# Kernel optimization log

Hardware: AMD Instinct MI355X
Metric: run time of the kernel (lower is better)

The kernel has to match this reference:

```python
import jax, jax.numpy as jnp
import numpy as np

N, C_IN, T, V = 64, 64, 64, 25
C_OUT = 64
DK = DV = 16
NH = 8
DKH, DVH = DK // NH, DV // NH
KT = 9
EPS = 1e-5


def make_pe(channel, joint_num, time_len):
    # temporal positional encoding: position index = frame id, repeated per joint
    pos = np.repeat(np.arange(time_len), joint_num).astype(np.float32)[:, None]
    pe = np.zeros((time_len * joint_num, channel), np.float32)
    div = np.exp(np.arange(0, channel, 2).astype(np.float32) * -(np.log(10000.0) / channel))
    pe[:, 0::2] = np.sin(pos * div)
    pe[:, 1::2] = np.cos(pos * div)
    return jnp.asarray(pe.reshape(time_len, joint_num, channel).transpose(2, 0, 1)[None])  # (1,C,time,joint)


def setup_inputs():
    key = jax.random.key(0)
    ks = jax.random.split(key, 17)
    rn = lambda k, s, sc=0.05: jax.random.normal(k, s, jnp.float32) * sc
    return {
        'x': jax.random.normal(ks[0], (N, C_IN, T, V), jnp.float32),
        'pe': make_pe(C_IN, V, 64),
        'data_bn_g': 1.0 + rn(ks[1], (C_IN * V,)),
        'data_bn_b': rn(ks[2], (C_IN * V,)),
        'qkv_w': rn(ks[3], (3 * DK + DV, C_IN), 0.1),
        'qkv_b': rn(ks[4], (3 * DK + DV,)),
        'attn_w': rn(ks[5], (DV, DV), 0.1),
        'attn_b': rn(ks[6], (DV,)),
        'tcn_w': rn(ks[7], (C_OUT - DV, C_IN, KT, 1), 0.05),
        'tcn_b': rn(ks[8], (C_OUT - DV,)),
        'tcn_bn_g': 1.0 + rn(ks[9], (C_OUT - DV,)),
        'tcn_bn_b': rn(ks[10], (C_OUT - DV,)),
        'fc1_w': rn(ks[11], (C_OUT // 2, C_OUT), 0.1),
        'fc1_b': rn(ks[12], (C_OUT // 2,)),
        'fc2_w': rn(ks[13], (C_OUT, C_OUT // 2), 0.1),
        'fc2_b': rn(ks[14], (C_OUT,)),
        'bn_g': 1.0 + rn(ks[15], (C_OUT,)),
        'bn_b': rn(ks[16], (C_OUT,)),
    }


def _bn_eval(x, g, b, axis=1):
    # eval-mode BatchNorm with running_mean=0, running_var=1
    shape = [1] * x.ndim
    shape[axis] = -1
    scale = g / jnp.sqrt(1.0 + EPS)
    return x * scale.reshape(shape) + b.reshape(shape)


def _qkv_heads(x2d, qkv_w, qkv_b):
    # x2d: (B, C, T); 1x1 conv == channel matmul; split q/k/g/v, g is projected but unused
    qkv = jnp.einsum('oc,bct->bot', qkv_w, x2d) + qkv_b[None, :, None]
    q, k, _g, v = jnp.split(qkv, [DK, 2 * DK, 3 * DK], axis=1)
    B = x2d.shape[0]
    split = lambda z, ch: z.reshape(B, NH, ch // NH, -1)  # (B, Nh, chh, T)
    q = split(q, DK) * (DKH ** -0.5)
    return q, split(k, DK), split(v, DV)


def reference(x, pe, data_bn_g, data_bn_b, qkv_w, qkv_b, attn_w, attn_b,
              tcn_w, tcn_b, tcn_bn_g, tcn_bn_b, fc1_w, fc1_b, fc2_w, fc2_b, bn_g, bn_b):
    y = x + pe[:, :, :T]                                 # positional encoding (N,C,T,V)
    x_sum = x
    # data_bn over flattened (C*V) channels
    xb = x.transpose(0, 1, 3, 2).reshape(N, C_IN * V, T)
    xb = _bn_eval(xb, data_bn_g, data_bn_b)
    xn = xb.reshape(N, C_IN, V, T).transpose(0, 1, 3, 2)  # (N,C,T,V)
    # fold joints into batch: (N*V, C, T)
    xf = xn.transpose(0, 3, 1, 2).reshape(N * V, C_IN, T)
    yf = y.transpose(0, 3, 1, 2).reshape(N * V, C_IN, T)
    fq, fk, fv = _qkv_heads(xf, qkv_w, qkv_b)
    pq, pk, _ = _qkv_heads(yf, qkv_w, qkv_b)
    mu_q = fq.mean(-1, keepdims=True)                     # (B,H,dkh,1)
    fqc = fq - mu_q
    logits_pos = jnp.einsum('bhcs,bhct->bhst', pq, pk)    # (B,H,T,T)
    pairwise = jnp.einsum('bhcs,bhct->bhst', fqc, fk)     # (B,H,T,T)
    unary = jnp.einsum('bhcs,bhct->bhst', mu_q, fk)       # (B,H,1,T)
    weights = jnp.tanh(pairwise + logits_pos) + jnp.tanh(unary + logits_pos)
    ao = jnp.einsum('bhst,bhct->bhsc', weights, fv)       # (B,H,T,dvh)
    # (B,H,1,T,dvh) -> permute(0,1,4,2,3) -> combine heads -> (B, DV, T)
    ao = ao.transpose(0, 1, 3, 2).reshape(N * V, DV, T)
    ao = jnp.einsum('oc,bct->bot', attn_w, ao) + attn_b[None, :, None]
    ao = ao.reshape(N, V, DV, T).transpose(0, 2, 3, 1)    # (N, DV, T, V)
    # temporal conv branch (Unit2D: conv(k=9 temporal) + eval BN)
    tc = jax.lax.conv_general_dilated(x_sum, tcn_w, (1, 1), ((KT // 2, KT // 2), (0, 0)),
                                      dimension_numbers=('NCHW', 'OIHW', 'NCHW'))
    tc = tc + tcn_b[None, :, None, None]
    tc = _bn_eval(tc, tcn_bn_g, tcn_bn_b)
    result = jnp.concatenate([tc, ao], axis=1) + x_sum    # residual (down is None)
    # SE-style channel gating
    se = result.mean(axis=(2, 3))                         # (N, C_OUT)
    gate = jax.nn.sigmoid(jax.nn.relu(se @ fc1_w.T + fc1_b) @ fc2_w.T + fc2_b)
    result = result * gate[:, :, None, None] + result
    result = _bn_eval(result, bn_g, bn_b)
    return jax.nn.relu(result)
```

## Files before the change

### kernel.cpp

```cpp
#include <hip/hip_runtime.h>
#include <hip/hip_bf16.h>
#include <math.h>

#define TV_ 1600
#define SCALE_K 2.885390081777927f
#define RS2_ 0.70710678118654752f

typedef __attribute__((ext_vector_type(8))) short bf16x8;
typedef __attribute__((ext_vector_type(4))) float f32x4;
typedef __attribute__((ext_vector_type(2))) __fp16 h2f;

union F4H { float4 f; h2f h[4]; };
union F2H { float2 f; h2f h[2]; };

__device__ __forceinline__ float tanh4(float y) {
    float e = __builtin_amdgcn_exp2f(y);
    float r = __builtin_amdgcn_rcpf(e + 1.f);
    return __builtin_fmaf(-2.f, r, 1.f);
}

__device__ __forceinline__ float dot2f(h2f a, h2f b, float c) {
    return __builtin_amdgcn_fdot2(a, b, c, false);
}

__device__ __forceinline__ ushort f2bf(float f) {
    __hip_bfloat16 h = __float2bfloat16(f);
    return *(ushort*)&h;
}
__device__ __forceinline__ float bf2f(ushort u) {
    uint w = ((uint)u) << 16;
    return __uint_as_float(w);
}

__global__ __launch_bounds__(256) void t1_kernel(
    const float* __restrict__ x, const float* __restrict__ pe,
    const float* __restrict__ tcn_w, const float* __restrict__ tg,
    const float* __restrict__ qkv_w, const float* __restrict__ qkv_b,
    const float* __restrict__ dbg, const float* __restrict__ dbb,
    ushort* __restrict__ rt, float* __restrict__ Sp, float* __restrict__ Tt,
    ushort* __restrict__ wb, ushort* __restrict__ wq, float* __restrict__ qb,
    ushort* __restrict__ pet, float* __restrict__ dbs)
{
    const int tid = threadIdx.x;
    const int bx = blockIdx.x, by = blockIdx.y;

    if (bx == 25) {
        #pragma unroll 1
        for (int j = 0; j < 9; ++j) {
            int idx = by * 256 + tid + j * 16384;
            if (idx < 27648) {
                int oc = idx / 576, kk = idx - oc * 576;
                int kt = kk >> 6, ci = kk & 63;
                float a = tg[oc] * rsqrtf(1.f + 1e-5f);
                wb[idx] = f2bf(tcn_w[(oc * 64 + ci) * 9 + kt] * a);
            } else if (idx < 32768) {
                int i2 = idx - 27648;
                int r = i2 >> 6, c = i2 & 63;
                int src; float sc;
                if (r < 16)      { src = r;      sc = RS2_; }
                else if (r < 32) { src = r;      sc = SCALE_K; }
                else if (r < 48) { src = r + 16; sc = 1.f; }
                else if (r < 64) { src = r - 48; sc = RS2_; }
                else             { src = r - 48; sc = SCALE_K; }
                wq[i2] = f2bf(qkv_w[src * 64 + c] * sc);
            } else if (idx < 32848) {
                int r = idx - 32768;
                int src; float sc;
                if (r < 16)      { src = r;      sc = RS2_; }
                else if (r < 32) { src = r;      sc = SCALE_K; }
                else if (r < 48) { src = r + 16; sc = 1.f; }
                else if (r < 64) { src = r - 48; sc = RS2_; }
                else             { src = r - 48; sc = SCALE_K; }
                qb[r] = qkv_b[src] * sc;
            } else if (idx < 135248) {
                int i3 = idx - 32848;
                int ci = i3 / 1600, tv = i3 - ci * 1600;
                pet[tv * 64 + ci] = f2bf(pe[ci * 1600 + tv]);
            } else if (idx < 138448) {
                int i4 = idx - 135248;
                int v = i4 >> 7, r = i4 & 127;
                if (r < 64) dbs[i4] = dbg[r * 25 + v] * rsqrtf(1.f + 1e-5f);
                else        dbs[i4] = dbb[(r - 64) * 25 + v];
            }
        }
        return;
    }
    if (bx == 26) {
        const int n = by;
        #pragma unroll
        for (int it = 0; it < 2; ++it) {
            int item = tid + it * 256;
            int ci = item >> 3, slot = item & 7;
            int t = (slot < 4) ? slot : (56 + slot);
            const float* xp = x + (n * 64 + ci) * TV_ + t * 25;
            float s = 0.f;
            #pragma unroll
            for (int v = 0; v < 25; ++v) s += xp[v];
            Tt[(n * 64 + ci) * 8 + slot] = s;
        }
        return;
    }

    __shared__ ushort smt[64 * 66];
    __shared__ float sps[64 * 65];
    const int tv0 = bx * 64;
    const int n = by;
    const int tvl = tid & 63, cig = tid >> 6;
    const int tv = tv0 + tvl;

    #pragma unroll
    for (int k = 0; k < 16; ++k) {
        int ci = cig * 16 + k;
        float xv = x[(n * 64 + ci) * TV_ + tv];
        smt[tvl * 66 + ci] = f2bf(xv);
        sps[ci * 65 + tvl] = xv;
    }
    __syncthreads();

    {
        const int c = tid >> 2, qr = tid & 3;
        float s = 0.f;
        #pragma unroll
        for (int i = 0; i < 16; ++i) s += sps[c * 65 + qr * 16 + i];
        s += __shfl_xor(s, 1);
        s += __shfl_xor(s, 2);
        if (qr == 0) Sp[(n * 25 + bx) * 64 + c] = s;
    }

    #pragma unroll
    for (int j = 0; j < 8; ++j) {
        int chunk = tid + j * 256;
        int tvr = chunk >> 5, p = chunk & 31;
        uint val = *(const uint*)&smt[tvr * 66 + p * 2];
        *(uint*)&rt[(n * TV_ + tv0 + tvr) * 64 + p * 2] = val;
    }
}

__global__ __launch_bounds__(256, 5) void score_kernel(
    const ushort* __restrict__ rt, const ushort* __restrict__ pet,
    const float* __restrict__ dbs,
    const ushort* __restrict__ wq, const float* __restrict__ qb,
    const float* __restrict__ attn_w, const float* __restrict__ attn_b,
    float* __restrict__ aoc, float* __restrict__ sep)
{
    __shared__ float sm[5856];
    ushort* smu = (ushort*)sm;
    const int MU_ = 1056;
    const int FK2 = 1120, PK2 = 1664, FV2 = 2208, PQ2 = 2752, FQ2 = 3296;
    const int AO2 = 3840;
    const int UN_ = 5312;

    const int b = blockIdx.x;
    const int l = b >> 3;
    const int n = (b & 7) * 8 + l / 25;
    const int v = l % 25;
    const int tid = threadIdx.x;

    const int lane = tid & 63, wave = tid >> 6;
    const int m16 = lane & 15, q = lane >> 4;

    {
        const int part = tid & 7;
        const int ci0 = part * 8;
        float sc8[8], sh8[8];
        *(float4*)&sc8[0] = *(const float4*)&dbs[v * 128 + ci0];
        *(float4*)&sc8[4] = *(const float4*)&dbs[v * 128 + ci0 + 4];
        *(float4*)&sh8[0] = *(const float4*)&dbs[v * 128 + 64 + ci0];
        *(float4*)&sh8[4] = *(const float4*)&dbs[v * 128 + 64 + ci0 + 4];
        #pragma unroll
        for (int j = 0; j < 2; ++j) {
            int t = (tid + j * 256) >> 3;
            uint4 xr = *(const uint4*)&rt[(n * TV_ + t * 25 + v) * 64 + ci0];
            uint4 pr = *(const uint4*)&pet[(t * 25 + v) * 64 + ci0];
            const ushort* xu = (const ushort*)&xr;
            const ushort* pu = (const ushort*)&pr;
            ushort xs[8], ys[8];
            #pragma unroll
            for (int i = 0; i < 8; ++i) {
                float xf = bf2f(xu[i]);
                xs[i] = f2bf(xf * sc8[i] + sh8[i]);
                ys[i] = f2bf(xf + bf2f(pu[i]));
            }
            *(uint4*)&smu[t * 72 + ci0] = *(uint4*)xs;
            *(uint4*)&smu[4608 + t * 72 + ci0] = *(uint4*)ys;
        }
    }
    __syncthreads();

    f32x4 acc[5];
    #pragma unroll
    for (int mt = 0; mt < 5; ++mt) acc[mt] = (f32x4){0.f, 0.f, 0.f, 0.f};
    #pragma unroll
    for (int kt = 0; kt < 2; ++kt) {
        const int koff = kt * 32 + q * 8;
        bf16x8 bx = *(const bf16x8*)&smu[(wave * 16 + m16) * 72 + koff];
        bf16x8 by = *(const bf16x8*)&smu[4608 + (wave * 16 + m16) * 72 + koff];
        #pragma unroll
        for (int mt = 0; mt < 5; ++mt) {
            bf16x8 a = *(const bf16x8*)&wq[(mt * 16 + m16) * 64 + koff];
            acc[mt] = __builtin_amdgcn_mfma_f32_16x16x32_bf16(a, (mt < 3) ? bx : by, acc[mt], 0, 0, 0);
        }
    }
    __syncthreads();

    {
        const int t = wave * 16 + m16;
        #pragma unroll
        for (int r = 0; r < 4; ++r)
            sm[(q * 4 + r) * 66 + t] = acc[0][r] + qb[q * 4 + r];
        const int p0 = (2 * q) * 68 + t, p1 = (2 * q + 1) * 68 + t;
        *(h2f*)&sm[FK2 + p0] = __builtin_amdgcn_cvt_pkrtz(acc[1][0] + qb[16 + 4 * q],     acc[1][1] + qb[16 + 4 * q + 1]);
        *(h2f*)&sm[FK2 + p1] = __builtin_amdgcn_cvt_pkrtz(acc[1][2] + qb[16 + 4 * q + 2], acc[1][3] + qb[16 + 4 * q + 3]);
        *(h2f*)&sm[FV2 + p0] = __builtin_amdgcn_cvt_pkrtz(acc[2][0] + qb[32 + 4 * q],     acc[2][1] + qb[32 + 4 * q + 1]);
        *(h2f*)&sm[FV2 + p1] = __builtin_amdgcn_cvt_pkrtz(acc[2][2] + qb[32 + 4 * q + 2], acc[2][3] + qb[32 + 4 * q + 3]);
        *(h2f*)&sm[PQ2 + p0] = __builtin_amdgcn_cvt_pkrtz(acc[3][0] + qb[48 + 4 * q],     acc[3][1] + qb[48 + 4 * q + 1]);
        *(h2f*)&sm[PQ2 + p1] = __builtin_amdgcn_cvt_pkrtz(acc[3][2] + qb[48 + 4 * q + 2], acc[3][3] + qb[48 + 4 * q + 3]);
        *(h2f*)&sm[PK2 + p0] = __builtin_amdgcn_cvt_pkrtz(acc[4][0] + qb[64 + 4 * q],     acc[4][1] + qb[64 + 4 * q + 1]);
        *(h2f*)&sm[PK2 + p1] = __builtin_amdgcn_cvt_pkrtz(acc[4][2] + qb[64 + 4 * q + 2], acc[4][3] + qb[64 + 4 * q + 3]);
    }
    __syncthreads();

    if (tid < 64) {
        int ch = tid & 15, qq = tid >> 4;
        float s = 0.f;
        #pragma unroll
        for (int t = 0; t < 16; ++t) s += sm[ch * 66 + qq * 16 + t];
        sm[MU_ + qq * 16 + ch] = s;
    }
    __syncthreads();
    if (tid < 16) {
        float mval = (sm[MU_ + tid] + sm[MU_ + 16 + tid] + sm[MU_ + 32 + tid] + sm[MU_ + 48 + tid]) * (1.f / 64.f);
        sm[MU_ + tid] = mval;
    }
    __syncthreads();

    #pragma unroll
    for (int e = 0; e < 2; ++e) {
        int idx = tid * 2 + e;
        int s = idx >> 3, h = idx & 7;
        float a = sm[(2 * h) * 66 + s] - sm[MU_ + 2 * h];
        float c = sm[(2 * h + 1) * 66 + s] - sm[MU_ + 2 * h + 1];
        *(h2f*)&sm[FQ2 + h * 68 + s] = __builtin_amdgcn_cvt_pkrtz(a, c);
    }
    {
        const int h = tid & 7, tt = tid >> 3;
        h2f mp = __builtin_amdgcn_cvt_pkrtz(sm[MU_ + 2 * h], sm[MU_ + 2 * h + 1]);
        sm[UN_ + h * 68 + tt]      = dot2f(mp, *(const h2f*)&sm[FK2 + h * 68 + tt], 0.f);
        sm[UN_ + h * 68 + tt + 32] = dot2f(mp, *(const h2f*)&sm[FK2 + h * 68 + tt + 32], 0.f);
    }
    __syncthreads();

    {
        const int h = tid & 7, sp = tid >> 3;
        const int hb = h * 68;
        F2H fqp, pqp;
        fqp.f = *(const float2*)&sm[FQ2 + hb + 2 * sp];
        pqp.f = *(const float2*)&sm[PQ2 + hb + 2 * sp];
        const h2f fq0 = fqp.h[0], fq1 = fqp.h[1];
        const h2f pq0 = pqp.h[0], pq1 = pqp.h[1];
        float ao00 = 0.f, ao01 = 0.f, ao10 = 0.f, ao11 = 0.f;
        #pragma unroll 2
        for (int t4 = 0; t4 < 16; ++t4) {
            F4H fk4, pk4, fv4;
            fk4.f = *(const float4*)&sm[FK2 + hb + 4 * t4];
            pk4.f = *(const float4*)&sm[PK2 + hb + 4 * t4];
            fv4.f = *(const float4*)&sm[FV2 + hb + 4 * t4];
            float4 un4 = *(const float4*)&sm[UN_ + hb + 4 * t4];
            const float* unp = (const float*)&un4;
            #pragma unroll
            for (int j = 0; j < 4; ++j) {
                float un = unp[j];
                float fva = (float)fv4.h[j].x, fvb = (float)fv4.h[j].y;
                float lp0 = dot2f(pq0, pk4.h[j], 0.f);
                float a10 = dot2f(fq0, fk4.h[j], lp0);
                float w0 = tanh4(a10) + tanh4(un + lp0);
                ao00 = __builtin_fmaf(w0, fva, ao00);
                ao01 = __builtin_fmaf(w0, fvb, ao01);
                float lp1 = dot2f(pq1, pk4.h[j], 0.f);
                float a11 = dot2f(fq1, fk4.h[j], lp1);
                float w1 = tanh4(a11) + tanh4(un + lp1);
                ao10 = __builtin_fmaf(w1, fva, ao10);
                ao11 = __builtin_fmaf(w1, fvb, ao11);
            }
        }
        *(float2*)&sm[AO2 + (2 * sp) * 20 + 2 * h]     = make_float2(ao00, ao01);
        *(float2*)&sm[AO2 + (2 * sp + 1) * 20 + 2 * h] = make_float2(ao10, ao11);
    }
    __syncthreads();

    const int t = tid & 63, oq = tid >> 6;
    float aorow[16];
    #pragma unroll
    for (int i = 0; i < 4; ++i)
        *(float4*)&aorow[i * 4] = *(const float4*)&sm[AO2 + t * 20 + i * 4];
    float* aop = aoc + (n * 25 + v) * 1024;
    #pragma unroll
    for (int j = 0; j < 4; ++j) {
        int o = oq * 4 + j;
        float acc4 = attn_b[o];
        #pragma unroll
        for (int c = 0; c < 16; ++c) acc4 += attn_w[o * 16 + c] * aorow[c];
        aop[o * 64 + t] = acc4;
        float ssum = acc4;
        #pragma unroll
        for (int off = 32; off >= 1; off >>= 1) ssum += __shfl_down(ssum, off, 64);
        if ((tid & 63) == 0) sep[(n * 25 + v) * 16 + o] = ssum;
    }
}

__global__ __launch_bounds__(256) void gate_kernel(
    const float* __restrict__ Sp, const float* __restrict__ Tt,
    const float* __restrict__ sep, const ushort* __restrict__ wb,
    const float* __restrict__ tcn_b, const float* __restrict__ tg,
    const float* __restrict__ tb,
    const float* __restrict__ fc1w, const float* __restrict__ fc1b,
    const float* __restrict__ fc2w, const float* __restrict__ fc2b,
    float* __restrict__ gateG)
{
    __shared__ float U[576];
    __shared__ float gp[432];
    __shared__ float SS[64], sepS[16], seL[64], hid[32];
    const int n = blockIdx.x;
    const int tid = threadIdx.x;
    const float rsbn = rsqrtf(1.f + 1e-5f);

    {
        const int c = tid >> 2, qr = tid & 3;
        float s = 0.f;
        #pragma unroll 1
        for (int j = qr; j < 25; j += 4) s += Sp[(n * 25 + j) * 64 + c];
        s += __shfl_xor(s, 1);
        s += __shfl_xor(s, 2);
        if (qr == 0) SS[c] = s;
    }
    if (tid < 64) {
        const int o = tid >> 2, qr = tid & 3;
        float s = 0.f;
        #pragma unroll 1
        for (int j = qr; j < 25; j += 4) s += sep[(n * 25 + j) * 16 + o];
        s += __shfl_xor(s, 1);
        s += __shfl_xor(s, 2);
        if (qr == 0) sepS[o] = s;
    }
    __syncthreads();
    if (tid < 64) {
        float S = SS[tid];
        float T[8];
        #pragma unroll
        for (int j = 0; j < 8; ++j) T[j] = Tt[(n * 64 + tid) * 8 + j];
        U[tid * 9 + 0] = S - (T[4] + T[5] + T[6] + T[7]);
        U[tid * 9 + 1] = S - (T[5] + T[6] + T[7]);
        U[tid * 9 + 2] = S - (T[6] + T[7]);
        U[tid * 9 + 3] = S - T[7];
        U[tid * 9 + 4] = S;
        U[tid * 9 + 5] = S - T[0];
        U[tid * 9 + 6] = S - (T[0] + T[1]);
        U[tid * 9 + 7] = S - (T[0] + T[1] + T[2]);
        U[tid * 9 + 8] = S - (T[0] + T[1] + T[2] + T[3]);
    }
    __syncthreads();
    if (tid < 432) {
        int oc = tid / 9, kt = tid - oc * 9;
        float cs = 0.f;
        #pragma unroll
        for (int cb = 0; cb < 8; ++cb) {
            bf16x8 w8 = *(const bf16x8*)&wb[oc * 576 + kt * 64 + cb * 8];
            #pragma unroll
            for (int i = 0; i < 8; ++i)
                cs += bf2f((ushort)w8[i]) * U[(cb * 8 + i) * 9 + kt];
        }
        gp[tid] = cs;
    }
    __syncthreads();
    if (tid < 64) {
        if (tid < 48) {
            float cs = 0.f;
            #pragma unroll
            for (int kt = 0; kt < 9; ++kt) cs += gp[tid * 9 + kt];
            float a = tg[tid] * rsbn;
            float cb_ = tcn_b[tid] * a + tb[tid];
            seL[tid] = (a * cs + 1600.f * cb_ + SS[tid]) * (1.f / 1600.f);
        } else {
            seL[tid] = (sepS[tid - 48] + SS[tid]) * (1.f / 1600.f);
        }
    }
    __syncthreads();
    if (tid < 32) {
        float a = fc1b[tid];
        #pragma unroll
        for (int c = 0; c < 64; ++c) a += fc1w[tid * 64 + c] * seL[c];
        hid[tid] = fmaxf(a, 0.f);
    }
    __syncthreads();
    if (tid < 64) {
        float g = fc2b[tid];
        #pragma unroll
        for (int j = 0; j < 32; ++j) g += fc2w[tid * 32 + j] * hid[j];
        gateG[n * 64 + tid] = 1.f / (1.f + __expf(-g));
    }
}

__global__ __launch_bounds__(512, 4) void tcn_mfma_kernel(
    const ushort* __restrict__ rt, const float* __restrict__ x,
    const ushort* __restrict__ wb,
    const float* __restrict__ tcn_b, const float* __restrict__ tg,
    const float* __restrict__ tb,
    const float* __restrict__ gateG, const float* __restrict__ aoc,
    const float* __restrict__ bng, const float* __restrict__ bnb,
    float* __restrict__ out)
{
    __shared__ ushort xsl[600 * 38];
    __shared__ float gateL[64];

    const int b = blockIdx.x;
    const int n = b >> 2, tile = b & 3;
    const int t0 = tile * 16;
    const int tid = threadIdx.x;
    const float rsbn = rsqrtf(1.f + 1e-5f);
    const int tvbase = (t0 - 4) * 25;

    if (tid < 64) gateL[tid] = gateG[n * 64 + tid];

    const int lane = tid & 63, wave = tid >> 6;
    const int m16 = lane & 15, q = lane >> 4;
    const int nt0 = wave * 3;

    f32x4 acc[3][3];
    f32x4 acc24[3];
    #pragma unroll
    for (int i = 0; i < 3; ++i)
        #pragma unroll
        for (int mt = 0; mt < 3; ++mt)
            acc[i][mt] = (f32x4){0.f, 0.f, 0.f, 0.f};
    #pragma unroll
    for (int mt = 0; mt < 3; ++mt) acc24[mt] = (f32x4){0.f, 0.f, 0.f, 0.f};

    #pragma unroll 1
    for (int hf = 0; hf < 2; ++hf) {
        if (hf) __syncthreads();
        for (int idx = tid; idx < 2400; idx += 512) {
            int r = idx >> 2, part = idx & 3;
            int tv = tvbase + r;
            uint4 val = make_uint4(0u, 0u, 0u, 0u);
            if (tv >= 0 && tv < TV_) val = *(const uint4*)&rt[(n * TV_ + tv) * 64 + hf * 32 + part * 8];
            *(uint4*)&xsl[r * 38 + part * 8] = val;
        }
        __syncthreads();
        #pragma unroll 1
        for (int kt = 0; kt < 9; ++kt) {
            const int ktile = kt * 2 + hf;
            bf16x8 afr[3];
            #pragma unroll
            for (int mt = 0; mt < 3; ++mt)
                afr[mt] = *(const bf16x8*)&wb[(mt * 16 + m16) * 576 + ktile * 32 + q * 8];
            #pragma unroll
            for (int i = 0; i < 3; ++i) {
                int p = (nt0 + i) * 16 + m16;
                bf16x8 bfr = *(const bf16x8*)&xsl[(p + kt * 25) * 38 + q * 8];
                #pragma unroll
                for (int mt = 0; mt < 3; ++mt)
                    acc[i][mt] = __builtin_amdgcn_mfma_f32_16x16x32_bf16(afr[mt], bfr, acc[i][mt], 0, 0, 0);
            }
            if (wave == 0) {
                int p = 24 * 16 + m16;
                bf16x8 bfr = *(const bf16x8*)&xsl[(p + kt * 25) * 38 + q * 8];
                #pragma unroll
                for (int mt = 0; mt < 3; ++mt)
                    acc24[mt] = __builtin_amdgcn_mfma_f32_16x16x32_bf16(afr[mt], bfr, acc24[mt], 0, 0, 0);
            }
        }
    }

    #pragma unroll
    for (int mt = 0; mt < 3; ++mt) {
        #pragma unroll
        for (int r = 0; r < 4; ++r) {
            int oc = mt * 16 + q * 4 + r;
            float a = tg[oc] * rsbn;
            float cb_ = tcn_b[oc] * a + tb[oc];
            float mm = (1.f + gateL[oc]) * (bng[oc] * rsbn);
            float bb = bnb[oc];
            #pragma unroll
            for (int i = 0; i < 3; ++i) {
                int posg = tile * 400 + (nt0 + i) * 16 + m16;
                float val = acc[i][mt][r] + cb_ + x[(n * 64 + oc) * TV_ + posg];
                out[(n * 64 + oc) * TV_ + posg] = fmaxf(val * mm + bb, 0.f);
            }
            if (wave == 0) {
                int posg = tile * 400 + 24 * 16 + m16;
                float val = acc24[mt][r] + cb_ + x[(n * 64 + oc) * TV_ + posg];
                out[(n * 64 + oc) * TV_ + posg] = fmaxf(val * mm + bb, 0.f);
            }
        }
    }

    __syncthreads();
    float* ts = (float*)xsl;
    for (int task = tid; task < 1600; task += 512) {
        int v = task >> 6;
        int r = task & 63;
        int o = r >> 2, f = r & 3;
        float4 d = *(const float4*)&aoc[(n * 25 + v) * 1024 + o * 64 + tile * 16 + f * 4];
        float* dst = &ts[v * 257 + o * 16 + f * 4];
        dst[0] = d.x; dst[1] = d.y; dst[2] = d.z; dst[3] = d.w;
    }
    __syncthreads();
    for (int p4 = tid; p4 < 1600; p4 += 512) {
        int o = p4 / 100, r4 = p4 - o * 100;
        int base4 = (n * 64 + 48 + o) * 400 + tile * 100 + r4;
        float4 xr = ((const float4*)x)[base4];
        float4 val;
        #pragma unroll
        for (int e = 0; e < 4; ++e) {
            int pos = r4 * 4 + e;
            int lt = pos / 25, v = pos - lt * 25;
            ((float*)&val)[e] = ts[v * 257 + o * 16 + lt];
        }
        float mm = (1.f + gateL[48 + o]) * (bng[48 + o] * rsbn);
        float bb = bnb[48 + o];
        val.x = fmaxf((val.x + xr.x) * mm + bb, 0.f);
        val.y = fmaxf((val.y + xr.y) * mm + bb, 0.f);
        val.z = fmaxf((val.z + xr.z) * mm + bb, 0.f);
        val.w = fmaxf((val.w + xr.w) * mm + bb, 0.f);
        ((float4*)out)[base4] = val;
    }
}

extern "C" void kernel_launch(void* const* d_in, const int* in_sizes, int n_in,
                              void* d_out, int out_size, void* d_ws, size_t ws_size,
                              hipStream_t stream) {
    const float* x     = (const float*)d_in[0];
    const float* pe    = (const float*)d_in[1];
    const float* dbg   = (const float*)d_in[2];
    const float* dbb   = (const float*)d_in[3];
    const float* qkvw  = (const float*)d_in[4];
    const float* qkvb  = (const float*)d_in[5];
    const float* attnw = (const float*)d_in[6];
    const float* attnb = (const float*)d_in[7];
    const float* tcnw  = (const float*)d_in[8];
    const float* tcnb  = (const float*)d_in[9];
    const float* tcng  = (const float*)d_in[10];
    const float* tcnbb = (const float*)d_in[11];
    const float* fc1w  = (const float*)d_in[12];
    const float* fc1b  = (const float*)d_in[13];
    const float* fc2w  = (const float*)d_in[14];
    const float* fc2b  = (const float*)d_in[15];
    const float* bng   = (const float*)d_in[16];
    const float* bnb   = (const float*)d_in[17];

    float* out  = (float*)d_out;
    float* Sp   = (float*)d_ws;
    float* sep  = Sp + 102400;
    float* Tt   = sep + 25600;
    float* qb   = Tt + 32768;
    float* aoc  = qb + 96;
    ushort* wb  = (ushort*)(aoc + 1638400);
    ushort* wq  = wb + 27648;
    ushort* pet = wq + 5120;
    ushort* rt  = pet + 102400;
    float* gateG = (float*)(rt + 6553600);
    float* dbs  = gateG + 4096;

    t1_kernel<<<dim3(27, 64), dim3(256), 0, stream>>>(
        x, pe, tcnw, tcng, qkvw, qkvb, dbg, dbb, rt, Sp, Tt, wb, wq, qb, pet, dbs);
    score_kernel<<<dim3(1600), dim3(256), 0, stream>>>(rt, pet, dbs, wq, qb, attnw, attnb, aoc, sep);
    gate_kernel<<<dim3(64), dim3(256), 0, stream>>>(
        Sp, Tt, sep, wb, tcnb, tcng, tcnbb, fc1w, fc1b, fc2w, fc2b, gateG);
    tcn_mfma_kernel<<<dim3(256), dim3(512), 0, stream>>>(
        rt, x, wb, tcnb, tcng, tcnbb, gateG, aoc, bng, bnb, out);
}
```

Before: 188.7 us.

## Split TCN tiles to 8 per sample and vectorize t1 input loads

The temporal-conv MFMA kernel now uses 8 tiles of 8 frames per sample instead of 4 tiles of 16. That doubles the grid to 512 blocks and shrinks the shared slab and per-wave accumulators, with waves covering 13 column tiles and the output masked to 200 positions. The aim is to fill more CUs on a 256-CU-class device, at the cost of a larger halo overhead (408 vs 200 rows loaded) and some idle waves. Separately, t1_kernel now loads x as float4 into a padded shared buffer instead of scalar loads, to cut global load instructions.

```diff
diff --git a/kernel.cpp b/kernel.cpp
--- a/kernel.cpp
+++ b/kernel.cpp
@@ -102,18 +102,20 @@
     }
 
     __shared__ ushort smt[64 * 66];
-    __shared__ float sps[64 * 65];
+    __shared__ float sps[64 * 68];
     const int tv0 = bx * 64;
     const int n = by;
-    const int tvl = tid & 63, cig = tid >> 6;
-    const int tv = tv0 + tvl;
-
-    #pragma unroll
-    for (int k = 0; k < 16; ++k) {
-        int ci = cig * 16 + k;
-        float xv = x[(n * 64 + ci) * TV_ + tv];
-        smt[tvl * 66 + ci] = f2bf(xv);
-        sps[ci * 65 + tvl] = xv;
+
+    #pragma unroll
+    for (int j = 0; j < 4; ++j) {
+        int f4 = tid + j * 256;
+        int ci = f4 >> 4, tv4 = f4 & 15;
+        float4 v4 = *(const float4*)&x[(n * 64 + ci) * TV_ + tv0 + tv4 * 4];
+        *(float4*)&sps[ci * 68 + tv4 * 4] = v4;
+        smt[(tv4 * 4 + 0) * 66 + ci] = f2bf(v4.x);
+        smt[(tv4 * 4 + 1) * 66 + ci] = f2bf(v4.y);
+        smt[(tv4 * 4 + 2) * 66 + ci] = f2bf(v4.z);
+        smt[(tv4 * 4 + 3) * 66 + ci] = f2bf(v4.w);
     }
     __syncthreads();
 
@@ -121,7 +123,7 @@
         const int c = tid >> 2, qr = tid & 3;
         float s = 0.f;
         #pragma unroll
-        for (int i = 0; i < 16; ++i) s += sps[c * 65 + qr * 16 + i];
+        for (int i = 0; i < 16; ++i) s += sps[c * 68 + qr * 16 + i];
         s += __shfl_xor(s, 1);
         s += __shfl_xor(s, 2);
         if (qr == 0) Sp[(n * 25 + bx) * 64 + c] = s;
@@ -400,7 +402,7 @@
     }
 }
 
-__global__ __launch_bounds__(512, 4) void tcn_mfma_kernel(
+__global__ __launch_bounds__(512, 2) void tcn_mfma_kernel(
     const ushort* __restrict__ rt, const float* __restrict__ x,
     const ushort* __restrict__ wb,
     const float* __restrict__ tcn_b, const float* __restrict__ tg,
@@ -409,36 +411,31 @@
     const float* __restrict__ bng, const float* __restrict__ bnb,
     float* __restrict__ out)
 {
-    __shared__ ushort xsl[600 * 38];
+    __shared__ ushort xsl[408 * 38];
     __shared__ float gateL[64];
 
     const int b = blockIdx.x;
-    const int n = b >> 2, tile = b & 3;
-    const int t0 = tile * 16;
+    const int n = b >> 3, tile = b & 7;
     const int tid = threadIdx.x;
     const float rsbn = rsqrtf(1.f + 1e-5f);
-    const int tvbase = (t0 - 4) * 25;
+    const int tvbase = tile * 200 - 100;
 
     if (tid < 64) gateL[tid] = gateG[n * 64 + tid];
 
     const int lane = tid & 63, wave = tid >> 6;
     const int m16 = lane & 15, q = lane >> 4;
-    const int nt0 = wave * 3;
-
-    f32x4 acc[3][3];
-    f32x4 acc24[3];
-    #pragma unroll
-    for (int i = 0; i < 3; ++i)
+
+    f32x4 acc[2][3];
+    #pragma unroll
+    for (int rr = 0; rr < 2; ++rr)
         #pragma unroll
         for (int mt = 0; mt < 3; ++mt)
-            acc[i][mt] = (f32x4){0.f, 0.f, 0.f, 0.f};
-    #pragma unroll
-    for (int mt = 0; mt < 3; ++mt) acc24[mt] = (f32x4){0.f, 0.f, 0.f, 0.f};
+            acc[rr][mt] = (f32x4){0.f, 0.f, 0.f, 0.f};
 
     #pragma unroll 1
     for (int hf = 0; hf < 2; ++hf) {
         if (hf) __syncthreads();
-        for (int idx = tid; idx < 2400; idx += 512) {
+        for (int idx = tid; idx < 1632; idx += 512) {
             int r = idx >> 2, part = idx & 3;
             int tv = tvbase + r;
             uint4 val = make_uint4(0u, 0u, 0u, 0u);
@@ -454,19 +451,15 @@
             for (int mt = 0; mt < 3; ++mt)
                 afr[mt] = *(const bf16x8*)&wb[(mt * 16 + m16) * 576 + ktile * 32 + q * 8];
             #pragma unroll
-            for (int i = 0; i < 3; ++i) {
-                int p = (nt0 + i) * 16 + m16;
-                bf16x8 bfr = *(const bf16x8*)&xsl[(p + kt * 25) * 38 + q * 8];
-                #pragma unroll
-                for (int mt = 0; mt < 3; ++mt)
-                    acc[i][mt] = __builtin_amdgcn_mfma_f32_16x16x32_bf16(afr[mt], bfr, acc[i][mt], 0, 0, 0);
-            }
-            if (wave == 0) {
-                int p = 24 * 16 + m16;
-                bf16x8 bfr = *(const bf16x8*)&xsl[(p + kt * 25) * 38 + q * 8];
-                #pragma unroll
-                for (int mt = 0; mt < 3; ++mt)
-                    acc24[mt] = __builtin_amdgcn_mfma_f32_16x16x32_bf16(afr[mt], bfr, acc24[mt], 0, 0, 0);
+            for (int rr = 0; rr < 2; ++rr) {
+                int w = wave + rr * 8;
+                if (w <= 12) {
+                    int p = w * 16 + m16;
+                    bf16x8 bfr = *(const bf16x8*)&xsl[(p + kt * 25) * 38 + q * 8];
+                    #pragma unroll
+                    for (int mt = 0; mt < 3; ++mt)
+                        acc[rr][mt] = __builtin_amdgcn_mfma_f32_16x16x32_bf16(afr[mt], bfr, acc[rr][mt], 0, 0, 0);
+                }
             }
         }
     }
@@ -481,40 +474,40 @@
             float mm = (1.f + gateL[oc]) * (bng[oc] * rsbn);
             float bb = bnb[oc];
             #pragma unroll
-            for (int i = 0; i < 3; ++i) {
-                int posg = tile * 400 + (nt0 + i) * 16 + m16;
-                float val = acc[i][mt][r] + cb_ + x[(n * 64 + oc) * TV_ + posg];
-                out[(n * 64 + oc) * TV_ + posg] = fmaxf(val * mm + bb, 0.f);
+            for (int rr = 0; rr < 2; ++rr) {
+                int w = wave + rr * 8;
+                if (w <= 12) {
+                    int p = w * 16 + m16;
+                    if (p < 200) {
+                        int posg = tile * 200 + p;
+                        float val = acc[rr][mt][r] + cb_ + x[(n * 64 + oc) * TV_ + posg];
+                        out[(n * 64 + oc) * TV_ + posg] = fmaxf(val * mm + bb, 0.f);
+                    }
+                }
             }
-            if (wave == 0) {
-                int posg = tile * 400 + 24 * 16 + m16;
-                float val = acc24[mt][r] + cb_ + x[(n * 64 + oc) * TV_ + posg];
-                out[(n * 64 + oc) * TV_ + posg] = fmaxf(val * mm + bb, 0.f);
-            }
         }
     }
 
     __syncthreads();
     float* ts = (float*)xsl;
-    for (int task = tid; task < 1600; task += 512) {
-        int v = task >> 6;
-        int r = task & 63;
-        int o = r >> 2, f = r & 3;
-        float4 d = *(const float4*)&aoc[(n * 25 + v) * 1024 + o * 64 + tile * 16 + f * 4];
-        float* dst = &ts[v * 257 + o * 16 + f * 4];
-        dst[0] = d.x; dst[1] = d.y; dst[2] = d.z; dst[3] = d.w;
-    }
-    __syncthreads();
-    for (int p4 = tid; p4 < 1600; p4 += 512) {
-        int o = p4 / 100, r4 = p4 - o * 100;
-        int base4 = (n * 64 + 48 + o) * 400 + tile * 100 + r4;
+    for (int task = tid; task < 800; task += 512) {
+        int v = task >> 5;
+        int r = task & 31;
+        int o = r >> 1, f = r & 1;
+        float4 d = *(const float4*)&aoc[(n * 25 + v) * 1024 + o * 64 + tile * 8 + f * 4];
+        *(float4*)&ts[v * 132 + o * 8 + f * 4] = d;
+    }
+    __syncthreads();
+    for (int p4 = tid; p4 < 800; p4 += 512) {
+        int o = p4 / 50, r4 = p4 - o * 50;
+        int base4 = (n * 64 + 48 + o) * 400 + tile * 50 + r4;
         float4 xr = ((const float4*)x)[base4];
         float4 val;
         #pragma unroll
         for (int e = 0; e < 4; ++e) {
             int pos = r4 * 4 + e;
             int lt = pos / 25, v = pos - lt * 25;
-            ((float*)&val)[e] = ts[v * 257 + o * 16 + lt];
+            ((float*)&val)[e] = ts[v * 132 + o * 8 + lt];
         }
         float mm = (1.f + gateL[48 + o]) * (bng[48 + o] * rsbn);
         float bb = bnb[48 + o];
@@ -566,6 +559,6 @@
     score_kernel<<<dim3(1600), dim3(256), 0, stream>>>(rt, pet, dbs, wq, qb, attnw, attnb, aoc, sep);
     gate_kernel<<<dim3(64), dim3(256), 0, stream>>>(
         Sp, Tt, sep, wb, tcnb, tcng, tcnbb, fc1w, fc1b, fc2w, fc2b, gateG);
-    tcn_mfma_kernel<<<dim3(256), dim3(512), 0, stream>>>(
+    tcn_mfma_kernel<<<dim3(512), dim3(512), 0, stream>>>(
         rt, x, wb, tcnb, tcng, tcnbb, gateG, aoc, bng, bnb, out);
 }
```

After: 204.8 us. 8.5% more time.
